# Kernel tuning notes

Hardware: AMD Instinct MI355X
Metric: run time of the kernel (lower is better)

Reference implementation:

```python
import jax, jax.numpy as jnp
import numpy as np

N_NODES = 8192
HIDDEN = 256
HEADS = 4
HEAD_DIM = HIDDEN // HEADS
NUM_EDGES = 4096
NUM_INC = 65536
LN_EPS = 1e-5


def setup_inputs() -> dict:
    key = jax.random.key(0)
    ks = jax.random.split(key, 8)
    scale = HIDDEN ** -0.5
    return {
        "x": jax.random.normal(ks[0], (N_NODES, HIDDEN), jnp.float32),
        "node_idx": jax.random.randint(ks[1], (NUM_INC,), 0, N_NODES),
        "edge_idx": jax.random.randint(ks[2], (NUM_INC,), 0, NUM_EDGES),
        "W_w": jax.random.normal(ks[3], (HIDDEN, HIDDEN), jnp.float32) * scale,
        "W_b": jax.random.normal(ks[4], (HIDDEN,), jnp.float32) * 0.02,
        "edge_att": jax.random.normal(ks[5], (HEADS, HEAD_DIM), jnp.float32) * scale,
        "out_w": jax.random.normal(ks[6], (HIDDEN, HIDDEN), jnp.float32) * scale,
        "out_b": jax.random.normal(ks[7], (HIDDEN,), jnp.float32) * 0.02,
    }


def reference(x, node_idx, edge_idx, W_w, W_b, edge_att, out_w, out_b):
    n = x.shape[0]
    e = node_idx.shape[0]
    # x' = W(x), split into heads: [N, heads, head_dim]
    xw = (x @ W_w.T + W_b).reshape(n, HEADS, HEAD_DIM)
    feat = xw[node_idx]                                   # [E, heads, hd]
    logits = jnp.einsum("ehd,hd->eh", feat, edge_att)      # [E, heads]
    # segment softmax over nodes within each hyperedge, per head
    seg_max = jax.ops.segment_max(logits, edge_idx, num_segments=NUM_EDGES)
    p = jnp.exp(logits - seg_max[edge_idx])
    seg_sum = jax.ops.segment_sum(p, edge_idx, num_segments=NUM_EDGES)
    attn = p / seg_sum[edge_idx]                           # [E, heads]
    attn_mean = attn.mean(axis=1)                          # mean over heads, [E]
    # hyperedges with < 2 nodes are skipped in the original
    sizes = jax.ops.segment_sum(jnp.ones((e,), x.dtype), edge_idx, num_segments=NUM_EDGES)
    valid = sizes[edge_idx] >= 2.0
    attn_mean = jnp.where(valid, attn_mean, 0.0)
    # scatter-add attention-weighted ORIGINAL features back to nodes
    contrib = attn_mean[:, None] * x[node_idx]             # [E, H]
    out = jnp.zeros_like(x).at[node_idx].add(contrib)
    # degree normalization counts ALL incidences (including size-1 edges)
    counts = jnp.zeros((n,), x.dtype).at[node_idx].add(1.0)
    out = out / jnp.clip(counts, 1.0)[:, None]
    out = out @ out_w.T + out_b
    # fresh nn.LayerNorm => affine identity, biased variance, eps=1e-5
    mu = out.mean(-1, keepdims=True)
    var = ((out - mu) ** 2).mean(-1, keepdims=True)
    out = (out - mu) / jnp.sqrt(var + LN_EPS)
    # NxN pairwise attention accumulation: AW[i,j] = sum_e attn_i(e)*count_j(e), diag zeroed
    A = jnp.zeros((n, NUM_EDGES), x.dtype).at[node_idx, edge_idx].add(attn_mean)
    B = jnp.zeros((n, NUM_EDGES), x.dtype).at[node_idx, edge_idx].add(1.0)
    attention_weights = A @ B.T
    attention_weights = attention_weights.at[jnp.diag_indices(n)].set(0.0)
    return out, attention_weights
```

## Files before the change

kernel.cpp:

```cpp
#include <hip/hip_runtime.h>
#include <stdint.h>

#define N_NODES  8192
#define HIDDEN   256
#define HEADS    4
#define HEAD_DIM 64
#define NUM_EDGES 4096
#define NUM_INC  65536
#define LN_EPS   1e-5f

typedef unsigned int uint_t;
typedef float __attribute__((ext_vector_type(4))) f4v;


#define OFF_SEGSZ    0
#define OFF_NCNT     16384
#define OFF_NFILL    49152
#define OFF_EFILL    81920
#define ZERO_BYTES   98304
#define OFF_VKH      98304
#define OFF_BL       102400
#define OFF_LOGIT    102464
#define OFF_NPTR     233536
#define OFF_EPTR     266320
#define OFF_SEGSUM   282720
#define OFF_NINC     348256
#define OFF_EMEM     610400
#define OFF_ITEM     872544

__global__ __launch_bounds__(256) void k_foldzero(const float* __restrict__ Ww,
                                                  const float* __restrict__ Wb,
                                                  const float* __restrict__ ea,
                                                  float* __restrict__ vkhT,
                                                  float* __restrict__ bl,
                                                  uint_t* __restrict__ zw) {
    int t = threadIdx.x, b = blockIdx.x;
    zw[b * 256 + t] = 0u;
    if (b < HEADS) {
        int k = t, h = b;
        float a = 0.f;
        for (int d = 0; d < HEAD_DIM; ++d)
            a += ea[h * HEAD_DIM + d] * Ww[(size_t)(h * HEAD_DIM + d) * HIDDEN + k];
        vkhT[h * HIDDEN + k] = a;
        if (k == 0) {
            float s = 0.f;
            for (int d = 0; d < HEAD_DIM; ++d)
                s += Wb[h * HEAD_DIM + d] * ea[h * HEAD_DIM + d];
            bl[h] = s;
        }
    }
}

__global__ __launch_bounds__(256) void k_logits(const float* __restrict__ x,
                                                const float* __restrict__ vkhT,
                                                const float* __restrict__ bl,
                                                float* __restrict__ logit) {
    __shared__ __align__(16) float xs[32 * HIDDEN];
    __shared__ __align__(16) float vs[HEADS * HIDDEN];
    __shared__ float bls[HEADS];
    int t = threadIdx.x, b = blockIdx.x;
    float4* xsv = (float4*)xs;
    const float4* xg = (const float4*)(x + (size_t)b * 32 * HIDDEN);
    #pragma unroll
    for (int i = 0; i < 8; ++i) xsv[i * 256 + t] = xg[i * 256 + t];
    ((float4*)vs)[t] = ((const float4*)vkhT)[t];
    if (t < HEADS) bls[t] = bl[t];
    __syncthreads();
    if (t < 128) {
        int n = t >> 2, h = t & 3;
        const float4* xr = (const float4*)(xs + n * HIDDEN);
        const float4* vr = (const float4*)(vs + h * HIDDEN);
        float acc = bls[h];
        for (int k4 = 0; k4 < HIDDEN / 4; ++k4) {
            float4 xv = xr[k4], vv = vr[k4];
            acc += xv.x * vv.x + xv.y * vv.y + xv.z * vv.z + xv.w * vv.w;
        }
        logit[(b * 32 + n) * HEADS + h] = acc;
    }
}

__global__ void k_pass1(const int* __restrict__ node_idx, const int* __restrict__ edge_idx,
                        int* __restrict__ seg_size, int* __restrict__ node_cnt) {
    int i = blockIdx.x * 256 + threadIdx.x;
    atomicAdd(&seg_size[edge_idx[i]], 1);
    atomicAdd(&node_cnt[node_idx[i]], 1);
}

__global__ __launch_bounds__(256) void k_scan(const int* __restrict__ node_cnt, int* __restrict__ node_ptr,
                                              const int* __restrict__ seg_size, int* __restrict__ edge_ptr) {
    __shared__ int part[256];
    const int* cnt; int* ptr; int n;
    if (blockIdx.x == 0) { cnt = node_cnt; ptr = node_ptr; n = N_NODES; }
    else                 { cnt = seg_size; ptr = edge_ptr; n = NUM_EDGES; }
    int t = threadIdx.x, C = n / 256;
    int s = 0;
    for (int j = 0; j < C; ++j) s += cnt[t * C + j];
    part[t] = s;
    __syncthreads();
    if (t == 0) {
        int run = 0;
        for (int i = 0; i < 256; ++i) { int tmp = part[i]; part[i] = run; run += tmp; }
        ptr[n] = run;
    }
    __syncthreads();
    int run = part[t];
    for (int j = 0; j < C; ++j) { ptr[t * C + j] = run; run += cnt[t * C + j]; }
}

__global__ void k_fill(const int* __restrict__ node_idx, const int* __restrict__ edge_idx,
                       const int* __restrict__ node_ptr, const int* __restrict__ edge_ptr,
                       int* __restrict__ node_fill, int* __restrict__ edge_fill,
                       int* __restrict__ node_inc, int* __restrict__ edge_mem) {
    int i = blockIdx.x * 256 + threadIdx.x;
    int n = node_idx[i], e = edge_idx[i];
    int p = node_ptr[n] + atomicAdd(&node_fill[n], 1);
    node_inc[p] = i;
    int q = edge_ptr[e] + atomicAdd(&edge_fill[e], 1);
    edge_mem[q] = n;
}

__global__ __launch_bounds__(256) void k_seg(const int* __restrict__ edge_ptr,
                                             const int* __restrict__ edge_mem,
                                             const float* __restrict__ logit,
                                             float* __restrict__ seg_sum) {
    int e = blockIdx.x * 256 + threadIdx.x;
    int qb = edge_ptr[e], qe = edge_ptr[e + 1];
    float s0 = 0, s1 = 0, s2 = 0, s3 = 0;
    for (int q = qb; q < qe; ++q) {
        int j = edge_mem[q];
        s0 += __expf(logit[j * 4 + 0]);
        s1 += __expf(logit[j * 4 + 1]);
        s2 += __expf(logit[j * 4 + 2]);
        s3 += __expf(logit[j * 4 + 3]);
    }
    seg_sum[e * 4 + 0] = s0; seg_sum[e * 4 + 1] = s1;
    seg_sum[e * 4 + 2] = s2; seg_sum[e * 4 + 3] = s3;
}

__global__ __launch_bounds__(256) void k_pairs(const int* __restrict__ node_inc,
                                               const int* __restrict__ node_idx,
                                               const int* __restrict__ edge_idx,
                                               const int* __restrict__ edge_ptr,
                                               const float* __restrict__ logit,
                                               const float* __restrict__ seg_sum,
                                               float4* __restrict__ item) {
    int p = blockIdx.x * 256 + threadIdx.x;
    int m = node_inc[p];
    int e = edge_idx[m];
    int qb = edge_ptr[e], qe = edge_ptr[e + 1];
    float a = 0.f;
    if (qe - qb >= 2) {
        int n = node_idx[m];
        float s = 0.f;
        #pragma unroll
        for (int h = 0; h < HEADS; ++h)
            s += __expf(logit[n * HEADS + h]) / seg_sum[e * HEADS + h];
        a = 0.25f * s;
    }
    float4 it;
    it.x = a;
    it.y = __int_as_float(qb);
    it.z = __int_as_float(qe);
    it.w = 0.f;
    item[p] = it;
}

__global__ __launch_bounds__(256) void k_aw_out(const float4* __restrict__ item,
                                                const int* __restrict__ node_ptr,
                                                const int* __restrict__ edge_mem,
                                                const float* __restrict__ x,
                                                const float* __restrict__ out_w,
                                                const float* __restrict__ out_b,
                                                float* __restrict__ AW,
                                                float* __restrict__ out0) {
    __shared__ __align__(16) float buf[N_NODES];
    __shared__ float sr[16], mu_s[16], rs_s[16];
    int t = threadIdx.x, w = t >> 6, lane = t & 63;
    int i = blockIdx.x;

    float4* rowv = (float4*)buf;
    #pragma unroll
    for (int c = 0; c < 8; ++c) rowv[c * 256 + t] = make_float4(0.f, 0.f, 0.f, 0.f);
    __syncthreads();
    int pb = node_ptr[i], pe = node_ptr[i + 1];
    for (int p = pb + w; p < pe; p += 4) {
        float4 it = item[p];
        float a = it.x;
        if (a != 0.f) {
            int qb = __float_as_int(it.y), qe = __float_as_int(it.z);
            for (int q = qb + lane; q < qe; q += 64)
                atomicAdd(&buf[edge_mem[q]], a);
        }
    }
    __syncthreads();
    if (t == 0) buf[i] = 0.f;
    __syncthreads();
    f4v* dst = (f4v*)(AW + (size_t)i * N_NODES);
    #pragma unroll
    for (int c = 0; c < 8; ++c)
        __builtin_nontemporal_store(((const f4v*)rowv)[c * 256 + t], &dst[c * 256 + t]);

    if (i >= 512) return;

    __syncthreads();
    float (*y)[260] = (float (*)[260])buf;
    int R = i * 16;
    if (t < 16) {
        int n = R + t;
        int nb = node_ptr[n], ne = node_ptr[n + 1];
        float ws = 0.f;
        for (int p = nb; p < ne; ++p) ws += item[p].x;
        int c = ne - nb; if (c < 1) c = 1;
        sr[t] = ws / (float)c;
    }
    __syncthreads();
    #pragma unroll
    for (int r = 0; r < 16; ++r)
        y[r][t] = sr[r] * x[(size_t)(R + r) * HIDDEN + t];
    __syncthreads();
    float acc[16];
    float bias = out_b[t];
    #pragma unroll
    for (int r = 0; r < 16; ++r) acc[r] = bias;
    const float4* wr4 = (const float4*)(out_w + (size_t)t * HIDDEN);
    for (int j4 = 0; j4 < HIDDEN / 4; ++j4) {
        float4 wv = wr4[j4];
        #pragma unroll
        for (int r = 0; r < 16; ++r) {
            float4 yv = *(const float4*)&y[r][j4 * 4];
            acc[r] += yv.x * wv.x + yv.y * wv.y + yv.z * wv.z + yv.w * wv.w;
        }
    }
    __syncthreads();
    #pragma unroll
    for (int r = 0; r < 16; ++r) y[r][t] = acc[r];
    __syncthreads();
    #pragma unroll
    for (int rr = 0; rr < 4; ++rr) {
        int r = (w << 2) | rr;
        float v = y[r][lane] + y[r][lane + 64] + y[r][lane + 128] + y[r][lane + 192];
        #pragma unroll
        for (int off = 32; off; off >>= 1) v += __shfl_down(v, off, 64);
        float mu = __shfl(v, 0, 64) * (1.0f / HIDDEN);
        float d0 = y[r][lane] - mu, d1 = y[r][lane + 64] - mu;
        float d2 = y[r][lane + 128] - mu, d3 = y[r][lane + 192] - mu;
        float s2 = d0 * d0 + d1 * d1 + d2 * d2 + d3 * d3;
        #pragma unroll
        for (int off = 32; off; off >>= 1) s2 += __shfl_down(s2, off, 64);
        if (lane == 0) {
            mu_s[r] = mu;
            rs_s[r] = rsqrtf(s2 * (1.0f / HIDDEN) + LN_EPS);
        }
    }
    __syncthreads();
    #pragma unroll
    for (int r = 0; r < 16; ++r)
        out0[(size_t)(R + r) * HIDDEN + t] = (y[r][t] - mu_s[r]) * rs_s[r];
}

extern "C" void kernel_launch(void* const* d_in, const int* in_sizes, int n_in,
                              void* d_out, int out_size, void* d_ws, size_t ws_size,
                              hipStream_t stream) {
    const float* x        = (const float*)d_in[0];
    const int*   node_idx = (const int*)d_in[1];
    const int*   edge_idx = (const int*)d_in[2];
    const float* Ww       = (const float*)d_in[3];
    const float* Wb       = (const float*)d_in[4];
    const float* ea       = (const float*)d_in[5];
    const float* ow       = (const float*)d_in[6];
    const float* ob       = (const float*)d_in[7];
    float* out0 = (float*)d_out;
    float* aw   = out0 + (size_t)N_NODES * HIDDEN;

    char* ws = (char*)d_ws;
    int*    seg_size  = (int*)(ws + OFF_SEGSZ);
    int*    node_cnt  = (int*)(ws + OFF_NCNT);
    int*    node_fill = (int*)(ws + OFF_NFILL);
    int*    edge_fill = (int*)(ws + OFF_EFILL);
    float*  vkhT      = (float*)(ws + OFF_VKH);
    float*  bl        = (float*)(ws + OFF_BL);
    float*  logit     = (float*)(ws + OFF_LOGIT);
    int*    node_ptr  = (int*)(ws + OFF_NPTR);
    int*    edge_ptr  = (int*)(ws + OFF_EPTR);
    float*  seg_sum   = (float*)(ws + OFF_SEGSUM);
    int*    node_inc  = (int*)(ws + OFF_NINC);
    int*    edge_mem  = (int*)(ws + OFF_EMEM);
    float4* item      = (float4*)(ws + OFF_ITEM);

    k_foldzero<<<ZERO_BYTES / 4 / 256, 256, 0, stream>>>(Ww, Wb, ea, vkhT, bl, (uint_t*)ws);
    k_logits<<<N_NODES / 32, 256, 0, stream>>>(x, vkhT, bl, logit);
    k_pass1<<<NUM_INC / 256, 256, 0, stream>>>(node_idx, edge_idx, seg_size, node_cnt);
    k_scan<<<2, 256, 0, stream>>>(node_cnt, node_ptr, seg_size, edge_ptr);
    k_fill<<<NUM_INC / 256, 256, 0, stream>>>(node_idx, edge_idx, node_ptr, edge_ptr,
                                              node_fill, edge_fill, node_inc, edge_mem);
    k_seg<<<NUM_EDGES / 256, 256, 0, stream>>>(edge_ptr, edge_mem, logit, seg_sum);
    k_pairs<<<NUM_INC / 256, 256, 0, stream>>>(node_inc, node_idx, edge_idx, edge_ptr,
                                               logit, seg_sum, item);
    k_aw_out<<<N_NODES, 256, 0, stream>>>(item, node_ptr, edge_mem, x, ow, ob, aw, out0);
}
```

Measured before the change: 368.3 us.

## Fuse preprocessing kernels into one cooperative kernel with grid syncs

Merges seven small preprocessing kernels (zeroing, logits, counting, scan, CSR fill, segment sums, pair items) into one cooperative kernel of 256 blocks separated by grid.sync barriers. The goal is to remove several kernel launches and the gaps between them on the stream. In exchange every phase now runs on a fixed 256-block grid, so the segment-sum phase uses only 16 threads per block and the scan uses only 2 blocks. Grid-wide barriers also have their own cost.

```diff
diff --git a/kernel.cpp b/kernel.cpp
--- a/kernel.cpp
+++ b/kernel.cpp
@@ -1,5 +1,8 @@
 #include <hip/hip_runtime.h>
+#include <hip/hip_cooperative_groups.h>
 #include <stdint.h>
+
+namespace cg = cooperative_groups;
 
 #define N_NODES  8192
 #define HIDDEN   256
@@ -28,14 +31,37 @@
 #define OFF_EMEM     610400
 #define OFF_ITEM     872544
 
-__global__ __launch_bounds__(256) void k_foldzero(const float* __restrict__ Ww,
-                                                  const float* __restrict__ Wb,
-                                                  const float* __restrict__ ea,
-                                                  float* __restrict__ vkhT,
-                                                  float* __restrict__ bl,
-                                                  uint_t* __restrict__ zw) {
+__global__ __launch_bounds__(256) void k_prep(
+    const float* __restrict__ x,
+    const int* __restrict__ node_idx,
+    const int* __restrict__ edge_idx,
+    const float* __restrict__ Ww,
+    const float* __restrict__ Wb,
+    const float* __restrict__ ea,
+    uint_t* __restrict__ ws_zero,
+    float* __restrict__ vkhT,
+    float* __restrict__ bl,
+    float* __restrict__ logit,
+    int* __restrict__ seg_size,
+    int* __restrict__ node_cnt,
+    int* __restrict__ node_ptr,
+    int* __restrict__ edge_ptr,
+    int* __restrict__ node_fill,
+    int* __restrict__ edge_fill,
+    int* __restrict__ node_inc,
+    int* __restrict__ edge_mem,
+    float* __restrict__ seg_sum,
+    float4* __restrict__ item)
+{
+    cg::grid_group grid = cg::this_grid();
     int t = threadIdx.x, b = blockIdx.x;
-    zw[b * 256 + t] = 0u;
+
+    __shared__ __align__(16) float xs[32 * HIDDEN];
+    __shared__ __align__(16) float vs[HEADS * HIDDEN];
+    __shared__ float bls[HEADS];
+    __shared__ int part[256];
+
+    if (t < 96) ws_zero[b * 96 + t] = 0u;
     if (b < HEADS) {
         int k = t, h = b;
         float a = 0.f;
@@ -49,120 +75,102 @@
             bl[h] = s;
         }
     }
-}
-
-__global__ __launch_bounds__(256) void k_logits(const float* __restrict__ x,
-                                                const float* __restrict__ vkhT,
-                                                const float* __restrict__ bl,
-                                                float* __restrict__ logit) {
-    __shared__ __align__(16) float xs[32 * HIDDEN];
-    __shared__ __align__(16) float vs[HEADS * HIDDEN];
-    __shared__ float bls[HEADS];
-    int t = threadIdx.x, b = blockIdx.x;
-    float4* xsv = (float4*)xs;
-    const float4* xg = (const float4*)(x + (size_t)b * 32 * HIDDEN);
-    #pragma unroll
-    for (int i = 0; i < 8; ++i) xsv[i * 256 + t] = xg[i * 256 + t];
-    ((float4*)vs)[t] = ((const float4*)vkhT)[t];
-    if (t < HEADS) bls[t] = bl[t];
-    __syncthreads();
-    if (t < 128) {
-        int n = t >> 2, h = t & 3;
-        const float4* xr = (const float4*)(xs + n * HIDDEN);
-        const float4* vr = (const float4*)(vs + h * HIDDEN);
-        float acc = bls[h];
-        for (int k4 = 0; k4 < HIDDEN / 4; ++k4) {
-            float4 xv = xr[k4], vv = vr[k4];
-            acc += xv.x * vv.x + xv.y * vv.y + xv.z * vv.z + xv.w * vv.w;
-        }
-        logit[(b * 32 + n) * HEADS + h] = acc;
-    }
-}
-
-__global__ void k_pass1(const int* __restrict__ node_idx, const int* __restrict__ edge_idx,
-                        int* __restrict__ seg_size, int* __restrict__ node_cnt) {
-    int i = blockIdx.x * 256 + threadIdx.x;
-    atomicAdd(&seg_size[edge_idx[i]], 1);
-    atomicAdd(&node_cnt[node_idx[i]], 1);
-}
-
-__global__ __launch_bounds__(256) void k_scan(const int* __restrict__ node_cnt, int* __restrict__ node_ptr,
-                                              const int* __restrict__ seg_size, int* __restrict__ edge_ptr) {
-    __shared__ int part[256];
-    const int* cnt; int* ptr; int n;
-    if (blockIdx.x == 0) { cnt = node_cnt; ptr = node_ptr; n = N_NODES; }
-    else                 { cnt = seg_size; ptr = edge_ptr; n = NUM_EDGES; }
-    int t = threadIdx.x, C = n / 256;
-    int s = 0;
-    for (int j = 0; j < C; ++j) s += cnt[t * C + j];
-    part[t] = s;
-    __syncthreads();
-    if (t == 0) {
-        int run = 0;
-        for (int i = 0; i < 256; ++i) { int tmp = part[i]; part[i] = run; run += tmp; }
-        ptr[n] = run;
-    }
-    __syncthreads();
-    int run = part[t];
-    for (int j = 0; j < C; ++j) { ptr[t * C + j] = run; run += cnt[t * C + j]; }
-}
-
-__global__ void k_fill(const int* __restrict__ node_idx, const int* __restrict__ edge_idx,
-                       const int* __restrict__ node_ptr, const int* __restrict__ edge_ptr,
-                       int* __restrict__ node_fill, int* __restrict__ edge_fill,
-                       int* __restrict__ node_inc, int* __restrict__ edge_mem) {
-    int i = blockIdx.x * 256 + threadIdx.x;
-    int n = node_idx[i], e = edge_idx[i];
-    int p = node_ptr[n] + atomicAdd(&node_fill[n], 1);
-    node_inc[p] = i;
-    int q = edge_ptr[e] + atomicAdd(&edge_fill[e], 1);
-    edge_mem[q] = n;
-}
-
-__global__ __launch_bounds__(256) void k_seg(const int* __restrict__ edge_ptr,
-                                             const int* __restrict__ edge_mem,
-                                             const float* __restrict__ logit,
-                                             float* __restrict__ seg_sum) {
-    int e = blockIdx.x * 256 + threadIdx.x;
-    int qb = edge_ptr[e], qe = edge_ptr[e + 1];
-    float s0 = 0, s1 = 0, s2 = 0, s3 = 0;
-    for (int q = qb; q < qe; ++q) {
-        int j = edge_mem[q];
-        s0 += __expf(logit[j * 4 + 0]);
-        s1 += __expf(logit[j * 4 + 1]);
-        s2 += __expf(logit[j * 4 + 2]);
-        s3 += __expf(logit[j * 4 + 3]);
-    }
-    seg_sum[e * 4 + 0] = s0; seg_sum[e * 4 + 1] = s1;
-    seg_sum[e * 4 + 2] = s2; seg_sum[e * 4 + 3] = s3;
-}
-
-__global__ __launch_bounds__(256) void k_pairs(const int* __restrict__ node_inc,
-                                               const int* __restrict__ node_idx,
-                                               const int* __restrict__ edge_idx,
-                                               const int* __restrict__ edge_ptr,
-                                               const float* __restrict__ logit,
-                                               const float* __restrict__ seg_sum,
-                                               float4* __restrict__ item) {
-    int p = blockIdx.x * 256 + threadIdx.x;
-    int m = node_inc[p];
-    int e = edge_idx[m];
-    int qb = edge_ptr[e], qe = edge_ptr[e + 1];
-    float a = 0.f;
-    if (qe - qb >= 2) {
-        int n = node_idx[m];
-        float s = 0.f;
+    grid.sync();
+
+    {
+        float4* xsv = (float4*)xs;
+        const float4* xg = (const float4*)(x + (size_t)b * 32 * HIDDEN);
         #pragma unroll
-        for (int h = 0; h < HEADS; ++h)
-            s += __expf(logit[n * HEADS + h]) / seg_sum[e * HEADS + h];
-        a = 0.25f * s;
-    }
-    float4 it;
-    it.x = a;
-    it.y = __int_as_float(qb);
-    it.z = __int_as_float(qe);
-    it.w = 0.f;
-    item[p] = it;
+        for (int i = 0; i < 8; ++i) xsv[i * 256 + t] = xg[i * 256 + t];
+        ((float4*)vs)[t] = ((const float4*)vkhT)[t];
+        if (t < HEADS) bls[t] = bl[t];
+        __syncthreads();
+        if (t < 128) {
+            int n = t >> 2, h = t & 3;
+            const float4* xr = (const float4*)(xs + n * HIDDEN);
+            const float4* vr = (const float4*)(vs + h * HIDDEN);
+            float acc = bls[h];
+            for (int k4 = 0; k4 < HIDDEN / 4; ++k4) {
+                float4 xv = xr[k4], vv = vr[k4];
+                acc += xv.x * vv.x + xv.y * vv.y + xv.z * vv.z + xv.w * vv.w;
+            }
+            logit[(b * 32 + n) * HEADS + h] = acc;
+        }
+    }
+    {
+        int i = b * 256 + t;
+        atomicAdd(&seg_size[edge_idx[i]], 1);
+        atomicAdd(&node_cnt[node_idx[i]], 1);
+    }
+    grid.sync();
+
+    if (b < 2) {
+        const int* cnt = (b == 0) ? node_cnt : seg_size;
+        int* ptr = (b == 0) ? node_ptr : edge_ptr;
+        int n = (b == 0) ? N_NODES : NUM_EDGES;
+        int C = n / 256;
+        int s = 0;
+        for (int j = 0; j < C; ++j) s += cnt[t * C + j];
+        part[t] = s;
+        __syncthreads();
+        if (t == 0) {
+            int run = 0;
+            for (int i = 0; i < 256; ++i) { int tmp = part[i]; part[i] = run; run += tmp; }
+            ptr[n] = run;
+        }
+        __syncthreads();
+        int run = part[t];
+        for (int j = 0; j < C; ++j) { ptr[t * C + j] = run; run += cnt[t * C + j]; }
+    }
+    grid.sync();
+
+    {
+        int i = b * 256 + t;
+        int n = node_idx[i], e = edge_idx[i];
+        int p = node_ptr[n] + atomicAdd(&node_fill[n], 1);
+        node_inc[p] = i;
+        int q = edge_ptr[e] + atomicAdd(&edge_fill[e], 1);
+        edge_mem[q] = n;
+    }
+    grid.sync();
+
+    if (t < 16) {
+        int e = b * 16 + t;
+        int qb = edge_ptr[e], qe = edge_ptr[e + 1];
+        float s0 = 0, s1 = 0, s2 = 0, s3 = 0;
+        for (int q = qb; q < qe; ++q) {
+            int j = edge_mem[q];
+            s0 += __expf(logit[j * 4 + 0]);
+            s1 += __expf(logit[j * 4 + 1]);
+            s2 += __expf(logit[j * 4 + 2]);
+            s3 += __expf(logit[j * 4 + 3]);
+        }
+        seg_sum[e * 4 + 0] = s0; seg_sum[e * 4 + 1] = s1;
+        seg_sum[e * 4 + 2] = s2; seg_sum[e * 4 + 3] = s3;
+    }
+    grid.sync();
+
+    {
+        int p = b * 256 + t;
+        int m = node_inc[p];
+        int e = edge_idx[m];
+        int qb = edge_ptr[e], qe = edge_ptr[e + 1];
+        float a = 0.f;
+        if (qe - qb >= 2) {
+            int n = node_idx[m];
+            float s = 0.f;
+            #pragma unroll
+            for (int h = 0; h < HEADS; ++h)
+                s += __expf(logit[n * HEADS + h]) / seg_sum[e * HEADS + h];
+            a = 0.25f * s;
+        }
+        float4 it;
+        it.x = a;
+        it.y = __int_as_float(qb);
+        it.z = __int_as_float(qe);
+        it.w = 0.f;
+        item[p] = it;
+    }
 }
 
 __global__ __launch_bounds__(256) void k_aw_out(const float4* __restrict__ item,
@@ -273,6 +281,7 @@
     float* aw   = out0 + (size_t)N_NODES * HIDDEN;
 
     char* ws = (char*)d_ws;
+    uint_t* ws_zero   = (uint_t*)ws;
     int*    seg_size  = (int*)(ws + OFF_SEGSZ);
     int*    node_cnt  = (int*)(ws + OFF_NCNT);
     int*    node_fill = (int*)(ws + OFF_NFILL);
@@ -287,14 +296,13 @@
     int*    edge_mem  = (int*)(ws + OFF_EMEM);
     float4* item      = (float4*)(ws + OFF_ITEM);
 
-    k_foldzero<<<ZERO_BYTES / 4 / 256, 256, 0, stream>>>(Ww, Wb, ea, vkhT, bl, (uint_t*)ws);
-    k_logits<<<N_NODES / 32, 256, 0, stream>>>(x, vkhT, bl, logit);
-    k_pass1<<<NUM_INC / 256, 256, 0, stream>>>(node_idx, edge_idx, seg_size, node_cnt);
-    k_scan<<<2, 256, 0, stream>>>(node_cnt, node_ptr, seg_size, edge_ptr);
-    k_fill<<<NUM_INC / 256, 256, 0, stream>>>(node_idx, edge_idx, node_ptr, edge_ptr,
-                                              node_fill, edge_fill, node_inc, edge_mem);
-    k_seg<<<NUM_EDGES / 256, 256, 0, stream>>>(edge_ptr, edge_mem, logit, seg_sum);
-    k_pairs<<<NUM_INC / 256, 256, 0, stream>>>(node_inc, node_idx, edge_idx, edge_ptr,
-                                               logit, seg_sum, item);
+    void* args[] = { (void*)&x, (void*)&node_idx, (void*)&edge_idx, (void*)&Ww,
+                     (void*)&Wb, (void*)&ea, (void*)&ws_zero, (void*)&vkhT,
+                     (void*)&bl, (void*)&logit, (void*)&seg_size, (void*)&node_cnt,
+                     (void*)&node_ptr, (void*)&edge_ptr, (void*)&node_fill,
+                     (void*)&edge_fill, (void*)&node_inc, (void*)&edge_mem,
+                     (void*)&seg_sum, (void*)&item };
+    hipLaunchCooperativeKernel((const void*)k_prep, dim3(256), dim3(256),
+                               args, 0, stream);
     k_aw_out<<<N_NODES, 256, 0, stream>>>(item, node_ptr, edge_mem, x, ow, ob, aw, out0);
 }
```

Result: slower. 497.3 us (+35.0%).
